# Performance work log

Hardware: AMD Instinct MI355X
Metric: run time of the kernel (lower is better)

Reference implementation:

```python
import jax, jax.numpy as jnp
import numpy as np


def setup_inputs() -> dict:
    key = jax.random.key(0)
    k1, k2, k3 = jax.random.split(key, 3)
    bsz, seqlen = 1024, 200
    vocab, d = 100000, 512
    xs = jax.random.randint(k1, (bsz, seqlen), 0, vocab, dtype=jnp.int64)
    lt_weight = jax.random.normal(k2, (vocab, d), dtype=jnp.float32)
    # freqs[i] = 1/(1+log(1+freq)) in the original -> positive weights in (0,1]
    freqs = jax.random.uniform(k3, (vocab,), dtype=jnp.float32, minval=0.05, maxval=1.0)
    return {"xs": xs, "lt_weight": lt_weight, "freqs": freqs}


def reference(xs, lt_weight, freqs):
    # embedding lookup: [bsz, len, d]
    xs_emb = lt_weight[xs]
    # vectorized replacement of the per-element python double loop:
    # x_scale[j, i] = freqs[xs[j, i]]  -> [bsz, len]
    x_scale = freqs[xs]
    # normalize by Frobenius norm of the whole [bsz, len] matrix (torch .norm())
    x_scale = x_scale / jnp.linalg.norm(x_scale)
    # weighted pooling: xs_emb^T @ x_scale -> [bsz, d]
    return jnp.einsum("bld,bl->bd", xs_emb, x_scale)
```

## Files before the change

### kernel.cpp

```cpp
#include <hip/hip_runtime.h>

#define SEQ 200
#define DIM 512

__global__ __launch_bounds__(256) void ssq_kernel(const int* __restrict__ xs,
                                                  const float* __restrict__ freqs,
                                                  double* __restrict__ ssq,
                                                  int n) {
    double acc = 0.0;
    for (int i = blockIdx.x * blockDim.x + threadIdx.x; i < n;
         i += gridDim.x * blockDim.x) {
        float f = freqs[xs[i]];
        acc += (double)f * (double)f;
    }
    for (int off = 32; off > 0; off >>= 1)
        acc += __shfl_down(acc, off, 64);
    __shared__ double s_w[4];
    int lane = threadIdx.x & 63;
    int wave = threadIdx.x >> 6;
    if (lane == 0) s_w[wave] = acc;
    __syncthreads();
    if (threadIdx.x == 0) {
        double t = s_w[0] + s_w[1] + s_w[2] + s_w[3];
        atomicAdd(ssq, t);
    }
}

__global__ __launch_bounds__(512) void pool_kernel(const int* __restrict__ xs,
                                                   const float* __restrict__ W,
                                                   const float* __restrict__ freqs,
                                                   const double* __restrict__ ssq,
                                                   float* __restrict__ out) {
    __shared__ int   s_idx[SEQ];
    __shared__ float s_scl[SEQ];
    __shared__ float s_part[3][DIM];

    const int b   = blockIdx.x;
    const int tid = threadIdx.x;

    const float inv_norm = (float)(1.0 / sqrt(ssq[0]));

    for (int l = tid; l < SEQ; l += 512) {
        int idx  = xs[b * SEQ + l];
        s_idx[l] = idx;
        s_scl[l] = freqs[idx] * inv_norm;
    }
    __syncthreads();

    const int group   = tid >> 7;
    const int lane128 = tid & 127;
    const int col4    = lane128 * 4;

    float4 acc = make_float4(0.f, 0.f, 0.f, 0.f);

    #pragma unroll 2
    for (int l = group; l < SEQ; l += 4) {
        const int   idx = s_idx[l];
        const float s   = s_scl[l];
        const float4 w  = *reinterpret_cast<const float4*>(
            W + (size_t)idx * DIM + col4);
        acc.x += s * w.x;
        acc.y += s * w.y;
        acc.z += s * w.z;
        acc.w += s * w.w;
    }

    if (group > 0)
        *reinterpret_cast<float4*>(&s_part[group - 1][col4]) = acc;
    __syncthreads();

    if (group == 0) {
        for (int g = 0; g < 3; ++g) {
            const float4 p = *reinterpret_cast<const float4*>(&s_part[g][col4]);
            acc.x += p.x; acc.y += p.y; acc.z += p.z; acc.w += p.w;
        }
        *reinterpret_cast<float4*>(out + (size_t)b * DIM + col4) = acc;
    }
}

extern "C" void kernel_launch(void* const* d_in, const int* in_sizes, int n_in,
                              void* d_out, int out_size, void* d_ws, size_t ws_size,
                              hipStream_t stream) {
    const int*   xs    = (const int*)d_in[0];
    const float* W     = (const float*)d_in[1];
    const float* freqs = (const float*)d_in[2];
    float* out = (float*)d_out;
    double* ssq = (double*)d_ws;

    const int n = in_sizes[0];
    const int bsz = n / SEQ;

    hipMemsetAsync(d_ws, 0, sizeof(double), stream);
    ssq_kernel<<<400, 256, 0, stream>>>(xs, freqs, ssq, n);
    pool_kernel<<<bsz, 512, 0, stream>>>(xs, W, freqs, ssq, out);
}
```

Baseline: 76.47 us.

## Fuse norm reduction and pooling into one cooperative kernel with grid sync

Replaces the separate sum-of-squares kernel and pooling kernel with a single cooperative kernel. Each of 512 blocks handles two batch rows, accumulates the squared frequencies while staging indices, pools unnormalized rows, then does a grid-wide sync and applies the inverse norm at the end. This removes one kernel launch and the second pass over xs and freqs. The costs are a grid barrier, the co-residency requirement for 512 blocks of 512 threads, and more registers for two accumulators. If the cooperative launch fails, it falls back to the old two-kernel path. The loop unroll also rises from 2 to 4.

```diff
diff --git a/kernel.cpp b/kernel.cpp
--- a/kernel.cpp
+++ b/kernel.cpp
@@ -1,7 +1,105 @@
 #include <hip/hip_runtime.h>
+#include <hip/hip_cooperative_groups.h>
 
-#define SEQ 200
-#define DIM 512
+namespace cg = cooperative_groups;
+
+#define SEQ  200
+#define DIM  512
+#define NBLK 512
+
+__global__ __launch_bounds__(512) void fused_kernel(const int* __restrict__ xs,
+                                                    const float* __restrict__ W,
+                                                    const float* __restrict__ freqs,
+                                                    double* __restrict__ ssq,
+                                                    float* __restrict__ out,
+                                                    int bsz) {
+    __shared__ int    s_idx[2][SEQ];
+    __shared__ float  s_f[2][SEQ];
+    __shared__ float  s_part[2][3][DIM];
+    __shared__ double s_w[8];
+    __shared__ float  s_inv;
+
+    const int tid     = threadIdx.x;
+    const int group   = tid >> 7;
+    const int lane128 = tid & 127;
+    const int col4    = lane128 * 4;
+
+    float ssl = 0.f;
+    for (int r = 0; r < 2; ++r) {
+        const int b = blockIdx.x + r * NBLK;
+        if (b < bsz) {
+            for (int l = tid; l < SEQ; l += 512) {
+                int   idx = xs[(size_t)b * SEQ + l];
+                float f   = freqs[idx];
+                s_idx[r][l] = idx;
+                s_f[r][l]   = f;
+                ssl += f * f;
+            }
+        }
+    }
+    double accd = (double)ssl;
+    for (int off = 32; off > 0; off >>= 1)
+        accd += __shfl_down(accd, off, 64);
+    const int lane = tid & 63, wave = tid >> 6;
+    if (lane == 0) s_w[wave] = accd;
+    __syncthreads();
+    if (tid == 0) {
+        double t = 0.0;
+        for (int w = 0; w < 8; ++w) t += s_w[w];
+        atomicAdd(ssq, t);
+    }
+
+    float4 acc[2];
+    for (int r = 0; r < 2; ++r) {
+        float4 a = make_float4(0.f, 0.f, 0.f, 0.f);
+        const int b = blockIdx.x + r * NBLK;
+        if (b < bsz) {
+            #pragma unroll 4
+            for (int l = group; l < SEQ; l += 4) {
+                const int   idx = s_idx[r][l];
+                const float s   = s_f[r][l];
+                const float4 w  = *reinterpret_cast<const float4*>(
+                    W + (size_t)idx * DIM + col4);
+                a.x += s * w.x;
+                a.y += s * w.y;
+                a.z += s * w.z;
+                a.w += s * w.w;
+            }
+        }
+        acc[r] = a;
+    }
+    if (group > 0) {
+        *reinterpret_cast<float4*>(&s_part[0][group - 1][col4]) = acc[0];
+        *reinterpret_cast<float4*>(&s_part[1][group - 1][col4]) = acc[1];
+    }
+    __syncthreads();
+    if (group == 0) {
+        for (int g = 0; g < 3; ++g) {
+            const float4 p0 = *reinterpret_cast<const float4*>(&s_part[0][g][col4]);
+            const float4 p1 = *reinterpret_cast<const float4*>(&s_part[1][g][col4]);
+            acc[0].x += p0.x; acc[0].y += p0.y; acc[0].z += p0.z; acc[0].w += p0.w;
+            acc[1].x += p1.x; acc[1].y += p1.y; acc[1].z += p1.z; acc[1].w += p1.w;
+        }
+    }
+
+    cg::this_grid().sync();
+    if (tid == 0) {
+        double v = __hip_atomic_load(ssq, __ATOMIC_ACQUIRE, __HIP_MEMORY_SCOPE_AGENT);
+        s_inv = (float)(1.0 / sqrt(v));
+    }
+    __syncthreads();
+    const float inv = s_inv;
+    if (group == 0) {
+        for (int r = 0; r < 2; ++r) {
+            const int b = blockIdx.x + r * NBLK;
+            if (b < bsz) {
+                float4 o = acc[r];
+                o.x *= inv; o.y *= inv; o.z *= inv; o.w *= inv;
+                *reinterpret_cast<float4*>(out + (size_t)b * DIM + col4) = o;
+            }
+        }
+    }
+}
 
 __global__ __launch_bounds__(256) void ssq_kernel(const int* __restrict__ xs,
                                                   const float* __restrict__ freqs,
@@ -16,14 +114,10 @@
     for (int off = 32; off > 0; off >>= 1)
         acc += __shfl_down(acc, off, 64);
     __shared__ double s_w[4];
-    int lane = threadIdx.x & 63;
-    int wave = threadIdx.x >> 6;
-    if (lane == 0) s_w[wave] = acc;
+    if ((threadIdx.x & 63) == 0) s_w[threadIdx.x >> 6] = acc;
     __syncthreads();
-    if (threadIdx.x == 0) {
-        double t = s_w[0] + s_w[1] + s_w[2] + s_w[3];
-        atomicAdd(ssq, t);
-    }
+    if (threadIdx.x == 0)
+        atomicAdd(ssq, s_w[0] + s_w[1] + s_w[2] + s_w[3]);
 }
 
 __global__ __launch_bounds__(512) void pool_kernel(const int* __restrict__ xs,
@@ -34,41 +128,28 @@
     __shared__ int   s_idx[SEQ];
     __shared__ float s_scl[SEQ];
     __shared__ float s_part[3][DIM];
-
     const int b   = blockIdx.x;
     const int tid = threadIdx.x;
-
     const float inv_norm = (float)(1.0 / sqrt(ssq[0]));
-
     for (int l = tid; l < SEQ; l += 512) {
-        int idx  = xs[b * SEQ + l];
+        int idx  = xs[(size_t)b * SEQ + l];
         s_idx[l] = idx;
         s_scl[l] = freqs[idx] * inv_norm;
     }
     __syncthreads();
-
-    const int group   = tid >> 7;
-    const int lane128 = tid & 127;
-    const int col4    = lane128 * 4;
-
+    const int group = tid >> 7, lane128 = tid & 127, col4 = lane128 * 4;
     float4 acc = make_float4(0.f, 0.f, 0.f, 0.f);
-
-    #pragma unroll 2
+    #pragma unroll 4
     for (int l = group; l < SEQ; l += 4) {
         const int   idx = s_idx[l];
         const float s   = s_scl[l];
         const float4 w  = *reinterpret_cast<const float4*>(
             W + (size_t)idx * DIM + col4);
-        acc.x += s * w.x;
-        acc.y += s * w.y;
-        acc.z += s * w.z;
-        acc.w += s * w.w;
+        acc.x += s * w.x; acc.y += s * w.y; acc.z += s * w.z; acc.w += s * w.w;
     }
-
     if (group > 0)
         *reinterpret_cast<float4*>(&s_part[group - 1][col4]) = acc;
     __syncthreads();
-
     if (group == 0) {
         for (int g = 0; g < 3; ++g) {
             const float4 p = *reinterpret_cast<const float4*>(&s_part[g][col4]);
@@ -84,13 +165,22 @@
     const int*   xs    = (const int*)d_in[0];
     const float* W     = (const float*)d_in[1];
     const float* freqs = (const float*)d_in[2];
-    float* out = (float*)d_out;
+    float*  out = (float*)d_out;
     double* ssq = (double*)d_ws;
 
-    const int n = in_sizes[0];
-    const int bsz = n / SEQ;
+    const int n   = in_sizes[0];
+    int bsz = n / SEQ;
 
     hipMemsetAsync(d_ws, 0, sizeof(double), stream);
-    ssq_kernel<<<400, 256, 0, stream>>>(xs, freqs, ssq, n);
-    pool_kernel<<<bsz, 512, 0, stream>>>(xs, W, freqs, ssq, out);
+
+    void* args[] = {(void*)&xs, (void*)&W, (void*)&freqs,
+                    (void*)&ssq, (void*)&out, (void*)&bsz};
+    hipError_t e = hipLaunchCooperativeKernel((const void*)fused_kernel,
+                                              dim3(NBLK), dim3(512),
+                                              args, 0, stream);
+    if (e != hipSuccess) {
+        (void)hipGetLastError();
+        ssq_kernel<<<400, 256, 0, stream>>>(xs, freqs, ssq, n);
+        pool_kernel<<<bsz, 512, 0, stream>>>(xs, W, freqs, ssq, out);
+    }
 }
```

Measured after the change: 145.4 us. +90.1%, slower.

## Replace atomic SSQ with per-block partials and batch gather loads

Applied to the files above, without the earlier changes.

Drops the memset and double-precision atomic by having each SSQ block write its own partial sum, which every pool block then reduces on its own. The per-thread SSQ accumulation moves from double to float. The pool loop now issues five independent float4 gathers before the FMAs to raise memory-level parallelism. The trade-off is a small redundant reduction in each of the 1024 pool blocks, an extra barrier, and slightly lower precision in the thread-local sum.

```diff
diff --git a/kernel.cpp b/kernel.cpp
--- a/kernel.cpp
+++ b/kernel.cpp
@@ -1,47 +1,57 @@
 #include <hip/hip_runtime.h>
 
-#define SEQ 200
-#define DIM 512
+#define SEQ        200
+#define DIM        512
+#define SSQ_BLOCKS 256
 
-__global__ __launch_bounds__(256) void ssq_kernel(const int* __restrict__ xs,
-                                                  const float* __restrict__ freqs,
-                                                  double* __restrict__ ssq,
-                                                  int n) {
-    double acc = 0.0;
-    for (int i = blockIdx.x * blockDim.x + threadIdx.x; i < n;
-         i += gridDim.x * blockDim.x) {
+__global__ __launch_bounds__(256) void ssq_partial(const int* __restrict__ xs,
+                                                   const float* __restrict__ freqs,
+                                                   double* __restrict__ partials,
+                                                   int n) {
+    float acc = 0.f;
+    for (int i = blockIdx.x * 256 + threadIdx.x; i < n; i += SSQ_BLOCKS * 256) {
         float f = freqs[xs[i]];
-        acc += (double)f * (double)f;
+        acc += f * f;
     }
+    double accd = (double)acc;
     for (int off = 32; off > 0; off >>= 1)
-        acc += __shfl_down(acc, off, 64);
+        accd += __shfl_down(accd, off, 64);
     __shared__ double s_w[4];
-    int lane = threadIdx.x & 63;
-    int wave = threadIdx.x >> 6;
-    if (lane == 0) s_w[wave] = acc;
+    if ((threadIdx.x & 63) == 0) s_w[threadIdx.x >> 6] = accd;
     __syncthreads();
-    if (threadIdx.x == 0) {
-        double t = s_w[0] + s_w[1] + s_w[2] + s_w[3];
-        atomicAdd(ssq, t);
-    }
+    if (threadIdx.x == 0)
+        partials[blockIdx.x] = s_w[0] + s_w[1] + s_w[2] + s_w[3];
 }
 
 __global__ __launch_bounds__(512) void pool_kernel(const int* __restrict__ xs,
                                                    const float* __restrict__ W,
                                                    const float* __restrict__ freqs,
-                                                   const double* __restrict__ ssq,
+                                                   const double* __restrict__ partials,
                                                    float* __restrict__ out) {
-    __shared__ int   s_idx[SEQ];
-    __shared__ float s_scl[SEQ];
-    __shared__ float s_part[3][DIM];
+    __shared__ int    s_idx[SEQ];
+    __shared__ float  s_scl[SEQ];
+    __shared__ float  s_part[3][DIM];
+    __shared__ double s_w[8];
+    __shared__ float  s_inv;
 
     const int b   = blockIdx.x;
     const int tid = threadIdx.x;
 
-    const float inv_norm = (float)(1.0 / sqrt(ssq[0]));
+    double v = (tid < SSQ_BLOCKS) ? partials[tid] : 0.0;
+    for (int off = 32; off > 0; off >>= 1)
+        v += __shfl_down(v, off, 64);
+    if ((tid & 63) == 0) s_w[tid >> 6] = v;
+    __syncthreads();
+    if (tid == 0) {
+        double t = 0.0;
+        for (int w = 0; w < 8; ++w) t += s_w[w];
+        s_inv = (float)(1.0 / sqrt(t));
+    }
+    __syncthreads();
+    const float inv_norm = s_inv;
 
     for (int l = tid; l < SEQ; l += 512) {
-        int idx  = xs[b * SEQ + l];
+        int idx  = xs[(size_t)b * SEQ + l];
         s_idx[l] = idx;
         s_scl[l] = freqs[idx] * inv_norm;
     }
@@ -53,22 +63,30 @@
 
     float4 acc = make_float4(0.f, 0.f, 0.f, 0.f);
 
-    #pragma unroll 2
-    for (int l = group; l < SEQ; l += 4) {
-        const int   idx = s_idx[l];
-        const float s   = s_scl[l];
-        const float4 w  = *reinterpret_cast<const float4*>(
-            W + (size_t)idx * DIM + col4);
-        acc.x += s * w.x;
-        acc.y += s * w.y;
-        acc.z += s * w.z;
-        acc.w += s * w.w;
+    #pragma unroll 1
+    for (int c = 0; c < SEQ / 4; c += 5) {
+        float4 wv[5];
+        float  sv[5];
+        #pragma unroll
+        for (int k = 0; k < 5; ++k) {
+            const int l = group + 4 * (c + k);
+            const int idx = s_idx[l];
+            sv[k] = s_scl[l];
+            wv[k] = *reinterpret_cast<const float4*>(
+                W + (size_t)idx * DIM + col4);
+        }
+        #pragma unroll
+        for (int k = 0; k < 5; ++k) {
+            acc.x += sv[k] * wv[k].x;
+            acc.y += sv[k] * wv[k].y;
+            acc.z += sv[k] * wv[k].z;
+            acc.w += sv[k] * wv[k].w;
+        }
     }
 
     if (group > 0)
         *reinterpret_cast<float4*>(&s_part[group - 1][col4]) = acc;
     __syncthreads();
-
     if (group == 0) {
         for (int g = 0; g < 3; ++g) {
             const float4 p = *reinterpret_cast<const float4*>(&s_part[g][col4]);
@@ -84,13 +102,12 @@
     const int*   xs    = (const int*)d_in[0];
     const float* W     = (const float*)d_in[1];
     const float* freqs = (const float*)d_in[2];
-    float* out = (float*)d_out;
-    double* ssq = (double*)d_ws;
+    float*  out      = (float*)d_out;
+    double* partials = (double*)d_ws;
 
-    const int n = in_sizes[0];
+    const int n   = in_sizes[0];
     const int bsz = n / SEQ;
 
-    hipMemsetAsync(d_ws, 0, sizeof(double), stream);
-    ssq_kernel<<<400, 256, 0, stream>>>(xs, freqs, ssq, n);
-    pool_kernel<<<bsz, 512, 0, stream>>>(xs, W, freqs, ssq, out);
+    ssq_partial<<<SSQ_BLOCKS, 256, 0, stream>>>(xs, freqs, partials, n);
+    pool_kernel<<<bsz, 512, 0, stream>>>(xs, W, freqs, partials, out);
 }
```

New measurement: 68.48 us. 1.12x faster.
